# Kernel tuning notes

Measured on AMD Instinct MI355X. Metric: run time of the kernel, lower is better.

## Reference

```python
import jax, jax.numpy as jnp
import numpy as np

N_LAYERS = 8
LAYER_NAMES = ['self', 'cross'] * 4
D_MODEL = 256
NHEAD = 8
HEAD_DIM = D_MODEL // NHEAD
EPS_ATTN = 1e-6
EPS_LN = 1e-5


def _xavier(key, shape):
    fan_in, fan_out = shape[-2], shape[-1]
    limit = float(np.sqrt(6.0 / (fan_in + fan_out)))
    return jax.random.uniform(key, shape, jnp.float32, -limit, limit)


def setup_inputs() -> dict:
    key = jax.random.key(0)
    ks = jax.random.split(key, 9)
    B, L, C = 4, 4800, D_MODEL
    inp = {
        'feat0': jax.random.normal(ks[0], (B, L, C), jnp.float32),
        'feat1': jax.random.normal(ks[1], (B, L, C), jnp.float32),
        # stacked per-layer params (layers are deepcopies, independently init'd)
        'Wq': _xavier(ks[2], (N_LAYERS, C, C)),
        'Wk': _xavier(ks[3], (N_LAYERS, C, C)),
        'Wv': _xavier(ks[4], (N_LAYERS, C, C)),
        'Wm': _xavier(ks[5], (N_LAYERS, C, C)),
        'W1': _xavier(ks[6], (N_LAYERS, 2 * C, 2 * C)),
        'W2': _xavier(ks[7], (N_LAYERS, 2 * C, C)),
        'ln1_w': jnp.ones((N_LAYERS, C), jnp.float32),
        'ln1_b': jnp.zeros((N_LAYERS, C), jnp.float32),
        'ln2_w': jnp.ones((N_LAYERS, C), jnp.float32),
        'ln2_b': jnp.zeros((N_LAYERS, C), jnp.float32),
    }
    return inp


def _layernorm(x, w, b):
    mu = jnp.mean(x, axis=-1, keepdims=True)
    var = jnp.mean(jnp.square(x - mu), axis=-1, keepdims=True)
    return (x - mu) * jax.lax.rsqrt(var + EPS_LN) * w + b


def _encoder_layer(x, source, Wq, Wk, Wv, Wm, W1, W2, ln1_w, ln1_b, ln2_w, ln2_b):
    bs, L, C = x.shape
    S = source.shape[1]
    q = (x @ Wq).reshape(bs, L, NHEAD, HEAD_DIM)
    k = (source @ Wk).reshape(bs, S, NHEAD, HEAD_DIM)
    v = (source @ Wv).reshape(bs, S, NHEAD, HEAD_DIM)
    # linear (kernelized) attention: phi(x) = elu(x) + 1
    Q = jax.nn.elu(q) + 1.0
    K = jax.nn.elu(k) + 1.0
    v_len = S
    v_scaled = v / v_len
    KV = jnp.einsum('nshd,nshv->nhdv', K, v_scaled)          # [N,H,D,D]
    Z = 1.0 / (jnp.einsum('nlhd,nhd->nlh', Q, K.sum(axis=1)) + EPS_ATTN)
    msg = jnp.einsum('nlhd,nhdv,nlh->nlhv', Q, KV, Z) * v_len  # [N,L,H,D]
    msg = msg.reshape(bs, L, C) @ Wm
    msg = _layernorm(msg, ln1_w, ln1_b)
    h = jnp.concatenate([x, msg], axis=-1)                   # [N,L,2C]
    h = jnp.maximum(h @ W1, 0.0) @ W2
    h = _layernorm(h, ln2_w, ln2_b)
    return x + h


def reference(feat0, feat1, Wq, Wk, Wv, Wm, W1, W2, ln1_w, ln1_b, ln2_w, ln2_b):
    for i, name in enumerate(LAYER_NAMES):
        p = (Wq[i], Wk[i], Wv[i], Wm[i], W1[i], W2[i],
             ln1_w[i], ln1_b[i], ln2_w[i], ln2_b[i])
        if name == 'self':
            feat0 = _encoder_layer(feat0, feat0, *p)
            feat1 = _encoder_layer(feat1, feat1, *p)
        else:  # cross
            feat0 = _encoder_layer(feat0, feat1, *p)
            feat1 = _encoder_layer(feat1, feat0, *p)
    return (feat0, feat1)
```

## Files before the change

### kernel.cpp

```cpp
#include <hip/hip_runtime.h>

typedef __attribute__((ext_vector_type(8))) short short8;
typedef __attribute__((ext_vector_type(4))) float f32x4;

#define DEV static __device__ __forceinline__

DEV unsigned short f2bf(float x) {
  union { float f; unsigned int u; } c; c.f = x;
  unsigned int r = c.u + 0x7fffu + ((c.u >> 16) & 1u);
  return (unsigned short)(r >> 16);
}
DEV float bf2f(unsigned short s) {
  union { unsigned int u; float f; } c; c.u = ((unsigned int)s) << 16;
  return c.f;
}
DEV float elu1(float x) { return x > 0.f ? x + 1.f : __expf(x); }

DEV void gload_lds16(const void* g, void* l) {
  __builtin_amdgcn_global_load_lds(
      (const __attribute__((address_space(1))) unsigned int*)g,
      (__attribute__((address_space(3))) unsigned int*)l, 16, 0, 0);
}

__global__ __launch_bounds__(256)
void wprep(const float* __restrict__ src, unsigned short* __restrict__ dst,
           int K, int N, int dls) {
  const int layer = blockIdx.z;
  src += (size_t)layer * K * N;
  dst += (size_t)layer * dls;
  __shared__ float tile[64][65];
  const int n0 = blockIdx.x * 64, k0 = blockIdx.y * 64;
  const int c = threadIdx.x & 63, r4 = threadIdx.x >> 6;
#pragma unroll
  for (int i = 0; i < 16; ++i) {
    int r = (i << 2) + r4;
    tile[r][c] = src[(size_t)(k0 + r) * N + n0 + c];
  }
  __syncthreads();
#pragma unroll
  for (int i = 0; i < 16; ++i) {
    int r = (i << 2) + r4;
    dst[(size_t)(n0 + r) * K + k0 + c] = f2bf(tile[c][r]);
  }
}

__global__ __launch_bounds__(256)
void cvt_bf16(const float* __restrict__ src, unsigned short* __restrict__ dst, int n4) {
  int i = blockIdx.x * 256 + threadIdx.x;
  if (i >= n4) return;
  float4 v = ((const float4*)src)[i];
  ushort4 o;
  o.x = f2bf(v.x); o.y = f2bf(v.y); o.z = f2bf(v.z); o.w = f2bf(v.w);
  ((ushort4*)dst)[i] = o;
}

template<int EPI>
__global__ __launch_bounds__(256)
void gemm_bt(const unsigned short* __restrict__ A0,
             const unsigned short* __restrict__ A1,
             const unsigned short* __restrict__ BT,
             float* __restrict__ Cf, unsigned short* __restrict__ Cb,
             int M, int N, int K, int lda) {
  __shared__ __align__(16) unsigned short As[128 * 64];
  __shared__ __align__(16) unsigned short Bs[128 * 64];
  const int tid = threadIdx.x;
  const int lane = tid & 63, wave = tid >> 6;
  const int tn = N >> 7;
  const int bm = (int)blockIdx.x / tn, bn = (int)blockIdx.x % tn;
  const int wm = (wave >> 1) << 6, wn = (wave & 1) << 6;
  const int lr = lane & 15, lk = lane >> 4;

  f32x4 acc[4][4];
#pragma unroll
  for (int i = 0; i < 4; ++i)
#pragma unroll
    for (int j = 0; j < 4; ++j) acc[i][j] = (f32x4){0.f, 0.f, 0.f, 0.f};

  for (int k0 = 0; k0 < K; k0 += 64) {
#pragma unroll
    for (int i = 0; i < 4; ++i) {
      const int cb = (i << 2) + wave;
      const int id = (cb << 6) + lane;
      const int row = id >> 3, ck = id & 7;
      const int gk = k0 + ((ck ^ (row & 7)) << 3);
      const unsigned short* srcA;
      if (A1) {
        srcA = (gk < 256) ? (A0 + (size_t)(bm * 128 + row) * 256 + gk)
                          : (A1 + (size_t)(bm * 128 + row) * 256 + (gk - 256));
      } else {
        srcA = A0 + (size_t)(bm * 128 + row) * lda + gk;
      }
      gload_lds16(srcA, As + (size_t)cb * 512);
      const unsigned short* srcB = BT + (size_t)(bn * 128 + row) * K + gk;
      gload_lds16(srcB, Bs + (size_t)cb * 512);
    }
    __syncthreads();
#pragma unroll
    for (int kk = 0; kk < 2; ++kk) {
      short8 af[4], bfr[4];
#pragma unroll
      for (int mi = 0; mi < 4; ++mi) {
        const int row = wm + mi * 16 + lr;
        const int ck = ((kk << 2) + lk) ^ (row & 7);
        af[mi] = *(const short8*)(As + row * 64 + ck * 8);
      }
#pragma unroll
      for (int ni = 0; ni < 4; ++ni) {
        const int row = wn + ni * 16 + lr;
        const int ck = ((kk << 2) + lk) ^ (row & 7);
        bfr[ni] = *(const short8*)(Bs + row * 64 + ck * 8);
      }
#pragma unroll
      for (int mi = 0; mi < 4; ++mi)
#pragma unroll
        for (int ni = 0; ni < 4; ++ni)
          acc[mi][ni] = __builtin_amdgcn_mfma_f32_16x16x32_bf16(af[mi], bfr[ni], acc[mi][ni], 0, 0, 0);
    }
    __syncthreads();
  }

  const int cr = lk << 2;
#pragma unroll
  for (int mi = 0; mi < 4; ++mi) {
#pragma unroll
    for (int ni = 0; ni < 4; ++ni) {
      const int colbase = bn * 128 + wn + ni * 16;
      const bool kside = colbase < 256;
#pragma unroll
      for (int j = 0; j < 4; ++j) {
        const int row = bm * 128 + wm + mi * 16 + cr + j;
        const int col = colbase + lr;
        float v = acc[mi][ni][j];
        if (EPI == 0) {
          Cf[(size_t)row * N + col] = v;
        } else if (EPI == 1) {
          Cb[(size_t)row * N + col] = f2bf(fmaxf(v, 0.f));
        } else if (EPI == 2) {
          Cf[(size_t)row * N + col] = kside ? elu1(v) : v;
        } else {
          Cb[(size_t)row * N + col] = f2bf(elu1(v));
        }
      }
    }
  }
}

__global__ __launch_bounds__(256)
void kv_partial(const float* __restrict__ kv, float* __restrict__ part) {
  const int ch = blockIdx.x, h = blockIdx.y, n = blockIdx.z;
  const int t = threadIdx.x, wave = t >> 6, lane = t & 63;
  __shared__ float kb[4][8][32];
  __shared__ float vb[4][8][32];
  const int dq = lane >> 3, vq = lane & 7;
  float a[4][4];
  float ks[4] = {0.f, 0.f, 0.f, 0.f};
#pragma unroll
  for (int i = 0; i < 4; ++i)
#pragma unroll
    for (int j = 0; j < 4; ++j) a[i][j] = 0.f;

  const int s_base = ch * 480 + wave * 120;
  for (int it = 0; it < 15; ++it) {
    __syncthreads();
#pragma unroll
    for (int i = 0; i < 2; ++i) {
      int f = i * 64 + lane;
      int r = f >> 4, c4 = f & 15;
      const float* gp = kv + ((size_t)(n * 4800 + s_base + it * 8 + r)) * 512 +
                        (c4 < 8 ? h * 32 + c4 * 4 : 256 + h * 32 + (c4 - 8) * 4);
      float4 val = *(const float4*)gp;
      if (c4 < 8) *(float4*)&kb[wave][r][c4 * 4] = val;
      else        *(float4*)&vb[wave][r][(c4 - 8) * 4] = val;
    }
    __syncthreads();
#pragma unroll
    for (int si = 0; si < 8; ++si) {
      float4 kq = *(const float4*)&kb[wave][si][dq * 4];
      float4 vv = *(const float4*)&vb[wave][si][vq * 4];
      ks[0] += kq.x; ks[1] += kq.y; ks[2] += kq.z; ks[3] += kq.w;
      a[0][0] += kq.x * vv.x; a[0][1] += kq.x * vv.y; a[0][2] += kq.x * vv.z; a[0][3] += kq.x * vv.w;
      a[1][0] += kq.y * vv.x; a[1][1] += kq.y * vv.y; a[1][2] += kq.y * vv.z; a[1][3] += kq.y * vv.w;
      a[2][0] += kq.z * vv.x; a[2][1] += kq.z * vv.y; a[2][2] += kq.z * vv.z; a[2][3] += kq.z * vv.w;
      a[3][0] += kq.w * vv.x; a[3][1] += kq.w * vv.y; a[3][2] += kq.w * vv.z; a[3][3] += kq.w * vv.w;
    }
  }
  float* pb = part + ((size_t)((n * 8 + h) * 40 + ch * 4 + wave)) * 1056;
#pragma unroll
  for (int i = 0; i < 4; ++i) {
#pragma unroll
    for (int j = 0; j < 4; ++j) pb[(dq * 4 + i) * 32 + vq * 4 + j] = a[i][j];
    if (vq == 0) pb[1024 + dq * 4 + i] = ks[i];
  }
}

__global__ __launch_bounds__(256)
void kv_reduce(const float* __restrict__ part, unsigned short* __restrict__ KVb,
               float* __restrict__ Ksum) {
  const int nh = blockIdx.x, t = threadIdx.x;
  const float* pb = part + (size_t)nh * 40 * 1056;
#pragma unroll
  for (int j = 0; j < 4; ++j) {
    int e = t * 4 + j;
    float s = 0.f;
    for (int c = 0; c < 40; ++c) s += pb[c * 1056 + e];
    int dd = e >> 5, vv = e & 31;
    size_t addr = ((size_t)(nh * 2 + (vv >> 4)) * 64 + ((dd >> 3) * 16 + (vv & 15))) * 8 + (dd & 7);
    KVb[addr] = f2bf(s);
  }
  if (t < 32) {
    float s = 0.f;
    for (int c = 0; c < 40; ++c) s += pb[c * 1056 + 1024 + t];
    Ksum[nh * 32 + t] = s;
  }
}

__global__ __launch_bounds__(256)
void msg_kernel(const unsigned short* __restrict__ qb, const unsigned short* __restrict__ KVb,
                const float* __restrict__ Ksum, unsigned short* __restrict__ msg) {
  const int n = blockIdx.y;
  const int wave = threadIdx.x >> 6, lane = threadIdx.x & 63;
  const int lr = lane & 15, lk = lane >> 4;
  const int lrow = blockIdx.x * 64 + wave * 16 + lr;
  const unsigned short* qrow = qb + ((size_t)n * 4800 + lrow) * 256;
  const short8* kvv = (const short8*)KVb;
  for (int h = 0; h < 8; ++h) {
    short8 af = *(const short8*)(qrow + h * 32 + lk * 8);
    const float* ksp = Ksum + (n * 8 + h) * 32 + lk * 8;
    float zp = 0.f;
#pragma unroll
    for (int j = 0; j < 8; ++j) zp += bf2f((unsigned short)af[j]) * ksp[j];
    zp += __shfl_xor(zp, 16);
    zp += __shfl_xor(zp, 32);
    float z = 1.f / (zp + 1e-6f);
    short8 b0 = kvv[((size_t)(n * 8 + h) * 2 + 0) * 64 + lane];
    short8 b1 = kvv[((size_t)(n * 8 + h) * 2 + 1) * 64 + lane];
    f32x4 acc0 = (f32x4){0.f, 0.f, 0.f, 0.f}, acc1 = (f32x4){0.f, 0.f, 0.f, 0.f};
    acc0 = __builtin_amdgcn_mfma_f32_16x16x32_bf16(af, b0, acc0, 0, 0, 0);
    acc1 = __builtin_amdgcn_mfma_f32_16x16x32_bf16(af, b1, acc1, 0, 0, 0);
#pragma unroll
    for (int j = 0; j < 4; ++j) {
      int rr = lk * 4 + j;
      float zj = __shfl(z, rr);
      int row = blockIdx.x * 64 + wave * 16 + rr;
      size_t base = ((size_t)n * 4800 + row) * 256 + h * 32;
      msg[base + lr] = f2bf(acc0[j] * zj);
      msg[base + 16 + lr] = f2bf(acc1[j] * zj);
    }
  }
}

template<int MODE>
__global__ __launch_bounds__(256)
void ln_kernel(const float* __restrict__ in, const float* __restrict__ xres,
               const float* __restrict__ w, const float* __restrict__ b,
               float* __restrict__ outf, unsigned short* __restrict__ outb) {
  const int wave = threadIdx.x >> 6, lane = threadIdx.x & 63;
  const size_t row = (size_t)blockIdx.x * 4 + wave;
  const float4 xv = ((const float4*)(in + row * 256))[lane];
  float s = xv.x + xv.y + xv.z + xv.w;
#pragma unroll
  for (int o = 1; o < 64; o <<= 1) s += __shfl_xor(s, o);
  const float mu = s * (1.f / 256.f);
  float d0 = xv.x - mu, d1 = xv.y - mu, d2 = xv.z - mu, d3 = xv.w - mu;
  float vs = d0 * d0 + d1 * d1 + d2 * d2 + d3 * d3;
#pragma unroll
  for (int o = 1; o < 64; o <<= 1) vs += __shfl_xor(vs, o);
  const float rstd = rsqrtf(vs * (1.f / 256.f) + 1e-5f);
  const float4 wv = ((const float4*)w)[lane];
  const float4 bv = ((const float4*)b)[lane];
  float y0 = d0 * rstd * wv.x + bv.x;
  float y1 = d1 * rstd * wv.y + bv.y;
  float y2 = d2 * rstd * wv.z + bv.z;
  float y3 = d3 * rstd * wv.w + bv.w;
  if (MODE == 0) {
    ushort4 o; o.x = f2bf(y0); o.y = f2bf(y1); o.z = f2bf(y2); o.w = f2bf(y3);
    ((ushort4*)(outb + row * 256))[lane] = o;
  } else {
    const float4 xr = ((const float4*)(xres + row * 256))[lane];
    float o0 = xr.x + y0, o1 = xr.y + y1, o2 = xr.z + y2, o3 = xr.w + y3;
    ((float4*)(outf + row * 256))[lane] = make_float4(o0, o1, o2, o3);
    ushort4 ob; ob.x = f2bf(o0); ob.y = f2bf(o1); ob.z = f2bf(o2); ob.w = f2bf(o3);
    ((ushort4*)(outb + row * 256))[lane] = ob;
  }
}

extern "C" void kernel_launch(void* const* d_in, const int* in_sizes, int n_in,
                              void* d_out, int out_size, void* d_ws, size_t ws_size,
                              hipStream_t stream) {
  (void)in_sizes; (void)n_in; (void)out_size; (void)ws_size;
  const float* feat0 = (const float*)d_in[0];
  const float* feat1 = (const float*)d_in[1];
  const float* Wq = (const float*)d_in[2];
  const float* Wk = (const float*)d_in[3];
  const float* Wv = (const float*)d_in[4];
  const float* Wm = (const float*)d_in[5];
  const float* W1 = (const float*)d_in[6];
  const float* W2 = (const float*)d_in[7];
  const float* ln1w = (const float*)d_in[8];
  const float* ln1b = (const float*)d_in[9];
  const float* ln2w = (const float*)d_in[10];
  const float* ln2b = (const float*)d_in[11];

  float* F0 = (float*)d_out;
  float* F1 = F0 + (size_t)4915200;

  size_t off = 0;
  auto alloc = [&](size_t bytes) -> void* {
    void* p = (char*)d_ws + off;
    off += (bytes + 255) & ~(size_t)255;
    return p;
  };
  unsigned short* qb     = (unsigned short*)alloc((size_t)19200 * 256 * 2);
  float*          kvbuf  = (float*)alloc((size_t)19200 * 512 * 4);
  unsigned short* msgb   = (unsigned short*)alloc((size_t)19200 * 256 * 2);
  unsigned short* msglnb = (unsigned short*)alloc((size_t)19200 * 256 * 2);
  unsigned short* F0b    = (unsigned short*)alloc((size_t)19200 * 256 * 2);
  unsigned short* F1b    = (unsigned short*)alloc((size_t)19200 * 256 * 2);
  float*          part   = (float*)alloc((size_t)32 * 40 * 1056 * 4);
  unsigned short* KVb    = (unsigned short*)alloc((size_t)32768 * 2);
  float*          Ksum   = (float*)alloc((size_t)1024 * 4);
  unsigned short* WqT    = (unsigned short*)alloc((size_t)8 * 65536 * 2);
  unsigned short* WkvT   = (unsigned short*)alloc((size_t)8 * 131072 * 2);
  unsigned short* WmT    = (unsigned short*)alloc((size_t)8 * 65536 * 2);
  unsigned short* W1T    = (unsigned short*)alloc((size_t)8 * 262144 * 2);
  unsigned short* W2T    = (unsigned short*)alloc((size_t)8 * 131072 * 2);
  float* mm = kvbuf;
  float* tt = kvbuf;
  unsigned short* h1b = (unsigned short*)(kvbuf + (size_t)19200 * 256);

  hipMemcpyAsync(F0, feat0, (size_t)4915200 * 4, hipMemcpyDeviceToDevice, stream);
  hipMemcpyAsync(F1, feat1, (size_t)4915200 * 4, hipMemcpyDeviceToDevice, stream);
  cvt_bf16<<<4800, 256, 0, stream>>>(feat0, F0b, 1228800);
  cvt_bf16<<<4800, 256, 0, stream>>>(feat1, F1b, 1228800);

  wprep<<<dim3(4, 4, 8), 256, 0, stream>>>(Wq, WqT, 256, 256, 65536);
  wprep<<<dim3(4, 4, 8), 256, 0, stream>>>(Wk, WkvT, 256, 256, 131072);
  wprep<<<dim3(4, 4, 8), 256, 0, stream>>>(Wv, WkvT + 65536, 256, 256, 131072);
  wprep<<<dim3(4, 4, 8), 256, 0, stream>>>(Wm, WmT, 256, 256, 65536);
  wprep<<<dim3(8, 8, 8), 256, 0, stream>>>(W1, W1T, 512, 512, 262144);
  wprep<<<dim3(4, 8, 8), 256, 0, stream>>>(W2, W2T, 512, 256, 131072);

  auto enc = [&](float* X, unsigned short* Xb, unsigned short* Sb, int i) {
    gemm_bt<3><<<300, 256, 0, stream>>>(Xb, nullptr, WqT + (size_t)i * 65536, nullptr, qb, 19200, 256, 256, 256);
    gemm_bt<2><<<600, 256, 0, stream>>>(Sb, nullptr, WkvT + (size_t)i * 131072, kvbuf, nullptr, 19200, 512, 256, 256);
    kv_partial<<<dim3(10, 8, 4), 256, 0, stream>>>(kvbuf, part);
    kv_reduce<<<32, 256, 0, stream>>>(part, KVb, Ksum);
    msg_kernel<<<dim3(75, 4), 256, 0, stream>>>(qb, KVb, Ksum, msgb);
    gemm_bt<0><<<300, 256, 0, stream>>>(msgb, nullptr, WmT + (size_t)i * 65536, mm, nullptr, 19200, 256, 256, 256);
    ln_kernel<0><<<4800, 256, 0, stream>>>(mm, nullptr, ln1w + i * 256, ln1b + i * 256, nullptr, msglnb);
    gemm_bt<1><<<600, 256, 0, stream>>>(Xb, msglnb, W1T + (size_t)i * 262144, nullptr, h1b, 19200, 512, 512, 256);
    gemm_bt<0><<<300, 256, 0, stream>>>(h1b, nullptr, W2T + (size_t)i * 131072, tt, nullptr, 19200, 256, 512, 512);
    ln_kernel<1><<<4800, 256, 0, stream>>>(tt, X, ln2w + i * 256, ln2b + i * 256, X, Xb);
  };

  for (int i = 0; i < 8; ++i) {
    if ((i & 1) == 0) { enc(F0, F0b, F0b, i); enc(F1, F1b, F1b, i); }
    else              { enc(F0, F0b, F1b, i); enc(F1, F1b, F0b, i); }
  }
}
```

Baseline: 2.021 ms.

## Fuse LayerNorm into GEMM epilogues, batch self layers, store K/V in bf16

Adds a gemm_ln kernel that computes a full 256-wide output row tile per block and applies LayerNorm (and the residual add) in the epilogue, which removes the separate ln kernels and the fp32 intermediate round-trips. Self-attention layers now process both feature maps in one batched pass with a fused QKV GEMM (N=768). K/V are stored as bf16 instead of fp32, and the initial memcpy is folded into the bf16 conversion kernel. The trade-offs are extra reduced precision in K/V, a one-pass variance formula (E[x²]−mu²) that can lose accuracy, and larger 512-thread blocks that lower the block count for the LN-fused GEMMs.

New measurement: 1.627 ms. 19.5% less time.

```diff
diff --git a/kernel.cpp b/kernel.cpp
--- a/kernel.cpp
+++ b/kernel.cpp
@@ -45,13 +45,15 @@
 }
 
 __global__ __launch_bounds__(256)
-void cvt_bf16(const float* __restrict__ src, unsigned short* __restrict__ dst, int n4) {
+void init_feat(const float* __restrict__ src, float* __restrict__ dstf,
+               unsigned short* __restrict__ dstb, int n4) {
   int i = blockIdx.x * 256 + threadIdx.x;
   if (i >= n4) return;
   float4 v = ((const float4*)src)[i];
+  ((float4*)dstf)[i] = v;
   ushort4 o;
   o.x = f2bf(v.x); o.y = f2bf(v.y); o.z = f2bf(v.z); o.w = f2bf(v.w);
-  ((ushort4*)dst)[i] = o;
+  ((ushort4*)dstb)[i] = o;
 }
 
 template<int EPI>
@@ -59,7 +61,7 @@
 void gemm_bt(const unsigned short* __restrict__ A0,
              const unsigned short* __restrict__ A1,
              const unsigned short* __restrict__ BT,
-             float* __restrict__ Cf, unsigned short* __restrict__ Cb,
+             unsigned short* __restrict__ Cb, unsigned short* __restrict__ Cb2,
              int M, int N, int K, int lda) {
   __shared__ __align__(16) unsigned short As[128 * 64];
   __shared__ __align__(16) unsigned short Bs[128 * 64];
@@ -125,32 +127,151 @@
 #pragma unroll
     for (int ni = 0; ni < 4; ++ni) {
       const int colbase = bn * 128 + wn + ni * 16;
-      const bool kside = colbase < 256;
 #pragma unroll
       for (int j = 0; j < 4; ++j) {
         const int row = bm * 128 + wm + mi * 16 + cr + j;
         const int col = colbase + lr;
         float v = acc[mi][ni][j];
-        if (EPI == 0) {
-          Cf[(size_t)row * N + col] = v;
-        } else if (EPI == 1) {
+        if (EPI == 1) {
           Cb[(size_t)row * N + col] = f2bf(fmaxf(v, 0.f));
         } else if (EPI == 2) {
-          Cf[(size_t)row * N + col] = kside ? elu1(v) : v;
+          Cb[(size_t)row * N + col] = f2bf(colbase < 256 ? elu1(v) : v);
+        } else if (EPI == 3) {
+          Cb[(size_t)row * 256 + col] = f2bf(elu1(v));
         } else {
-          Cb[(size_t)row * N + col] = f2bf(elu1(v));
+          if (colbase < 256) Cb[(size_t)row * 256 + col] = f2bf(elu1(v));
+          else Cb2[(size_t)row * 512 + (col - 256)] = f2bf(colbase < 512 ? elu1(v) : v);
         }
       }
     }
   }
 }
 
-__global__ __launch_bounds__(256)
-void kv_partial(const float* __restrict__ kv, float* __restrict__ part) {
+template<int EPI>
+__global__ __launch_bounds__(512)
+void gemm_ln(const unsigned short* __restrict__ A, const unsigned short* __restrict__ BT,
+             const float* __restrict__ lnw, const float* __restrict__ lnb,
+             const float* __restrict__ xres, float* __restrict__ outf,
+             unsigned short* __restrict__ outb, int K) {
+  __shared__ __align__(16) unsigned short As[128 * 64];
+  __shared__ __align__(16) unsigned short Bs[256 * 64];
+  const int tid = threadIdx.x;
+  const int lane = tid & 63, wid = tid >> 6;
+  const int bm = blockIdx.x;
+  const int wm = (wid >> 2) << 6, wn = (wid & 3) << 6;
+  const int lr = lane & 15, lk = lane >> 4;
+
+  f32x4 acc[4][4];
+#pragma unroll
+  for (int i = 0; i < 4; ++i)
+#pragma unroll
+    for (int j = 0; j < 4; ++j) acc[i][j] = (f32x4){0.f, 0.f, 0.f, 0.f};
+
+  for (int k0 = 0; k0 < K; k0 += 64) {
+#pragma unroll
+    for (int i = 0; i < 2; ++i) {
+      const int cb = i * 8 + wid;
+      const int id = (cb << 6) + lane;
+      const int row = id >> 3, ck = id & 7;
+      const int gk = k0 + ((ck ^ (row & 7)) << 3);
+      gload_lds16(A + (size_t)(bm * 128 + row) * K + gk, As + (size_t)cb * 512);
+    }
+#pragma unroll
+    for (int i = 0; i < 4; ++i) {
+      const int cb = i * 8 + wid;
+      const int id = (cb << 6) + lane;
+      const int row = id >> 3, ck = id & 7;
+      const int gk = k0 + ((ck ^ (row & 7)) << 3);
+      gload_lds16(BT + (size_t)row * K + gk, Bs + (size_t)cb * 512);
+    }
+    __syncthreads();
+#pragma unroll
+    for (int kk = 0; kk < 2; ++kk) {
+      short8 af[4], bfr[4];
+#pragma unroll
+      for (int mi = 0; mi < 4; ++mi) {
+        const int row = wm + mi * 16 + lr;
+        const int ck = ((kk << 2) + lk) ^ (row & 7);
+        af[mi] = *(const short8*)(As + row * 64 + ck * 8);
+      }
+#pragma unroll
+      for (int ni = 0; ni < 4; ++ni) {
+        const int row = wn + ni * 16 + lr;
+        const int ck = ((kk << 2) + lk) ^ (row & 7);
+        bfr[ni] = *(const short8*)(Bs + row * 64 + ck * 8);
+      }
+#pragma unroll
+      for (int mi = 0; mi < 4; ++mi)
+#pragma unroll
+        for (int ni = 0; ni < 4; ++ni)
+          acc[mi][ni] = __builtin_amdgcn_mfma_f32_16x16x32_bf16(af[mi], bfr[ni], acc[mi][ni], 0, 0, 0);
+    }
+    __syncthreads();
+  }
+
+  float* red = (float*)As;
+  float wv[4], bv[4];
+#pragma unroll
+  for (int ni = 0; ni < 4; ++ni) {
+    wv[ni] = lnw[wn + ni * 16 + lr];
+    bv[ni] = lnb[wn + ni * 16 + lr];
+  }
+#pragma unroll
+  for (int mi = 0; mi < 4; ++mi) {
+#pragma unroll
+    for (int j = 0; j < 4; ++j) {
+      float s = 0.f, q = 0.f;
+#pragma unroll
+      for (int ni = 0; ni < 4; ++ni) {
+        float v = acc[mi][ni][j];
+        s += v; q += v * v;
+      }
+#pragma unroll
+      for (int o = 1; o < 16; o <<= 1) {
+        s += __shfl_xor(s, o);
+        q += __shfl_xor(q, o);
+      }
+      if (lr == 0) {
+        int row = wm + mi * 16 + (lk << 2) + j;
+        red[row * 8 + (wid & 3) * 2] = s;
+        red[row * 8 + (wid & 3) * 2 + 1] = q;
+      }
+    }
+  }
+  __syncthreads();
+#pragma unroll
+  for (int mi = 0; mi < 4; ++mi) {
+#pragma unroll
+    for (int j = 0; j < 4; ++j) {
+      const int row = wm + mi * 16 + (lk << 2) + j;
+      const size_t grow = (size_t)bm * 128 + row;
+      float s = red[row * 8] + red[row * 8 + 2] + red[row * 8 + 4] + red[row * 8 + 6];
+      float q = red[row * 8 + 1] + red[row * 8 + 3] + red[row * 8 + 5] + red[row * 8 + 7];
+      float mu = s * (1.f / 256.f);
+      float var = q * (1.f / 256.f) - mu * mu;
+      float rstd = rsqrtf(var + 1e-5f);
+#pragma unroll
+      for (int ni = 0; ni < 4; ++ni) {
+        int col = wn + ni * 16 + lr;
+        float y = (acc[mi][ni][j] - mu) * rstd * wv[ni] + bv[ni];
+        if (EPI == 0) {
+          outb[grow * 256 + col] = f2bf(y);
+        } else {
+          float o = xres[grow * 256 + col] + y;
+          outf[grow * 256 + col] = o;
+          outb[grow * 256 + col] = f2bf(o);
+        }
+      }
+    }
+  }
+}
+
+__global__ __launch_bounds__(256)
+void kv_partial(const unsigned short* __restrict__ kvb, float* __restrict__ part) {
   const int ch = blockIdx.x, h = blockIdx.y, n = blockIdx.z;
   const int t = threadIdx.x, wave = t >> 6, lane = t & 63;
-  __shared__ float kb[4][8][32];
-  __shared__ float vb[4][8][32];
+  __shared__ float kb[4][8][36];
+  __shared__ float vb[4][8][36];
   const int dq = lane >> 3, vq = lane & 7;
   float a[4][4];
   float ks[4] = {0.f, 0.f, 0.f, 0.f};
@@ -160,18 +281,16 @@
     for (int j = 0; j < 4; ++j) a[i][j] = 0.f;
 
   const int s_base = ch * 480 + wave * 120;
+  const int half = lane >> 5, l = lane & 31, r = l >> 2, c8 = l & 3;
+  const unsigned short* src = kvb + ((size_t)n * 4800 + s_base + r) * 512 +
+                              half * 256 + h * 32 + c8 * 8;
+  float* dst = (half ? &vb[wave][r][0] : &kb[wave][r][0]) + c8 * 8;
+
   for (int it = 0; it < 15; ++it) {
     __syncthreads();
-#pragma unroll
-    for (int i = 0; i < 2; ++i) {
-      int f = i * 64 + lane;
-      int r = f >> 4, c4 = f & 15;
-      const float* gp = kv + ((size_t)(n * 4800 + s_base + it * 8 + r)) * 512 +
-                        (c4 < 8 ? h * 32 + c4 * 4 : 256 + h * 32 + (c4 - 8) * 4);
-      float4 val = *(const float4*)gp;
-      if (c4 < 8) *(float4*)&kb[wave][r][c4 * 4] = val;
-      else        *(float4*)&vb[wave][r][(c4 - 8) * 4] = val;
-    }
+    short8 raw = *(const short8*)(src + (size_t)it * 8 * 512);
+#pragma unroll
+    for (int e = 0; e < 8; ++e) dst[e] = bf2f((unsigned short)raw[e]);
     __syncthreads();
 #pragma unroll
     for (int si = 0; si < 8; ++si) {
@@ -246,41 +365,6 @@
       msg[base + lr] = f2bf(acc0[j] * zj);
       msg[base + 16 + lr] = f2bf(acc1[j] * zj);
     }
-  }
-}
-
-template<int MODE>
-__global__ __launch_bounds__(256)
-void ln_kernel(const float* __restrict__ in, const float* __restrict__ xres,
-               const float* __restrict__ w, const float* __restrict__ b,
-               float* __restrict__ outf, unsigned short* __restrict__ outb) {
-  const int wave = threadIdx.x >> 6, lane = threadIdx.x & 63;
-  const size_t row = (size_t)blockIdx.x * 4 + wave;
-  const float4 xv = ((const float4*)(in + row * 256))[lane];
-  float s = xv.x + xv.y + xv.z + xv.w;
-#pragma unroll
-  for (int o = 1; o < 64; o <<= 1) s += __shfl_xor(s, o);
-  const float mu = s * (1.f / 256.f);
-  float d0 = xv.x - mu, d1 = xv.y - mu, d2 = xv.z - mu, d3 = xv.w - mu;
-  float vs = d0 * d0 + d1 * d1 + d2 * d2 + d3 * d3;
-#pragma unroll
-  for (int o = 1; o < 64; o <<= 1) vs += __shfl_xor(vs, o);
-  const float rstd = rsqrtf(vs * (1.f / 256.f) + 1e-5f);
-  const float4 wv = ((const float4*)w)[lane];
-  const float4 bv = ((const float4*)b)[lane];
-  float y0 = d0 * rstd * wv.x + bv.x;
-  float y1 = d1 * rstd * wv.y + bv.y;
-  float y2 = d2 * rstd * wv.z + bv.z;
-  float y3 = d3 * rstd * wv.w + bv.w;
-  if (MODE == 0) {
-    ushort4 o; o.x = f2bf(y0); o.y = f2bf(y1); o.z = f2bf(y2); o.w = f2bf(y3);
-    ((ushort4*)(outb + row * 256))[lane] = o;
-  } else {
-    const float4 xr = ((const float4*)(xres + row * 256))[lane];
-    float o0 = xr.x + y0, o1 = xr.y + y1, o2 = xr.z + y2, o3 = xr.w + y3;
-    ((float4*)(outf + row * 256))[lane] = make_float4(o0, o1, o2, o3);
-    ushort4 ob; ob.x = f2bf(o0); ob.y = f2bf(o1); ob.z = f2bf(o2); ob.w = f2bf(o3);
-    ((ushort4*)(outb + row * 256))[lane] = ob;
   }
 }
 
@@ -310,51 +394,72 @@
     off += (bytes + 255) & ~(size_t)255;
     return p;
   };
-  unsigned short* qb     = (unsigned short*)alloc((size_t)19200 * 256 * 2);
-  float*          kvbuf  = (float*)alloc((size_t)19200 * 512 * 4);
-  unsigned short* msgb   = (unsigned short*)alloc((size_t)19200 * 256 * 2);
-  unsigned short* msglnb = (unsigned short*)alloc((size_t)19200 * 256 * 2);
-  unsigned short* F0b    = (unsigned short*)alloc((size_t)19200 * 256 * 2);
-  unsigned short* F1b    = (unsigned short*)alloc((size_t)19200 * 256 * 2);
-  float*          part   = (float*)alloc((size_t)32 * 40 * 1056 * 4);
-  unsigned short* KVb    = (unsigned short*)alloc((size_t)32768 * 2);
-  float*          Ksum   = (float*)alloc((size_t)1024 * 4);
-  unsigned short* WqT    = (unsigned short*)alloc((size_t)8 * 65536 * 2);
-  unsigned short* WkvT   = (unsigned short*)alloc((size_t)8 * 131072 * 2);
+  unsigned short* Fb     = (unsigned short*)alloc((size_t)38400 * 256 * 2);
+  unsigned short* qb     = (unsigned short*)alloc((size_t)38400 * 256 * 2);
+  unsigned short* kvb    = (unsigned short*)alloc((size_t)38400 * 512 * 2);
+  unsigned short* msgb   = (unsigned short*)alloc((size_t)38400 * 256 * 2);
+  unsigned short* msglnb = (unsigned short*)alloc((size_t)38400 * 256 * 2);
+  float*          part   = (float*)alloc((size_t)64 * 40 * 1056 * 4);
+  unsigned short* KVb    = (unsigned short*)alloc((size_t)65536 * 2);
+  float*          Ksum   = (float*)alloc((size_t)2048 * 4);
+  unsigned short* WqkvT  = (unsigned short*)alloc((size_t)8 * 196608 * 2);
   unsigned short* WmT    = (unsigned short*)alloc((size_t)8 * 65536 * 2);
   unsigned short* W1T    = (unsigned short*)alloc((size_t)8 * 262144 * 2);
   unsigned short* W2T    = (unsigned short*)alloc((size_t)8 * 131072 * 2);
-  float* mm = kvbuf;
-  float* tt = kvbuf;
-  unsigned short* h1b = (unsigned short*)(kvbuf + (size_t)19200 * 256);
-
-  hipMemcpyAsync(F0, feat0, (size_t)4915200 * 4, hipMemcpyDeviceToDevice, stream);
-  hipMemcpyAsync(F1, feat1, (size_t)4915200 * 4, hipMemcpyDeviceToDevice, stream);
-  cvt_bf16<<<4800, 256, 0, stream>>>(feat0, F0b, 1228800);
-  cvt_bf16<<<4800, 256, 0, stream>>>(feat1, F1b, 1228800);
-
-  wprep<<<dim3(4, 4, 8), 256, 0, stream>>>(Wq, WqT, 256, 256, 65536);
-  wprep<<<dim3(4, 4, 8), 256, 0, stream>>>(Wk, WkvT, 256, 256, 131072);
-  wprep<<<dim3(4, 4, 8), 256, 0, stream>>>(Wv, WkvT + 65536, 256, 256, 131072);
+  unsigned short* h1b = kvb;
+  unsigned short* F0b = Fb;
+  unsigned short* F1b = Fb + (size_t)19200 * 256;
+
+  init_feat<<<4800, 256, 0, stream>>>(feat0, F0, F0b, 1228800);
+  init_feat<<<4800, 256, 0, stream>>>(feat1, F1, F1b, 1228800);
+
+  wprep<<<dim3(4, 4, 8), 256, 0, stream>>>(Wq, WqkvT, 256, 256, 196608);
+  wprep<<<dim3(4, 4, 8), 256, 0, stream>>>(Wk, WqkvT + 65536, 256, 256, 196608);
+  wprep<<<dim3(4, 4, 8), 256, 0, stream>>>(Wv, WqkvT + 131072, 256, 256, 196608);
   wprep<<<dim3(4, 4, 8), 256, 0, stream>>>(Wm, WmT, 256, 256, 65536);
   wprep<<<dim3(8, 8, 8), 256, 0, stream>>>(W1, W1T, 512, 512, 262144);
   wprep<<<dim3(4, 8, 8), 256, 0, stream>>>(W2, W2T, 512, 256, 131072);
 
-  auto enc = [&](float* X, unsigned short* Xb, unsigned short* Sb, int i) {
-    gemm_bt<3><<<300, 256, 0, stream>>>(Xb, nullptr, WqT + (size_t)i * 65536, nullptr, qb, 19200, 256, 256, 256);
-    gemm_bt<2><<<600, 256, 0, stream>>>(Sb, nullptr, WkvT + (size_t)i * 131072, kvbuf, nullptr, 19200, 512, 256, 256);
-    kv_partial<<<dim3(10, 8, 4), 256, 0, stream>>>(kvbuf, part);
+  auto enc_self = [&](int i) {
+    gemm_bt<4><<<1800, 256, 0, stream>>>(Fb, nullptr, WqkvT + (size_t)i * 196608,
+                                         qb, kvb, 38400, 768, 256, 256);
+    kv_partial<<<dim3(10, 8, 8), 256, 0, stream>>>(kvb, part);
+    kv_reduce<<<64, 256, 0, stream>>>(part, KVb, Ksum);
+    msg_kernel<<<dim3(75, 8), 256, 0, stream>>>(qb, KVb, Ksum, msgb);
+    gemm_ln<0><<<300, 512, 0, stream>>>(msgb, WmT + (size_t)i * 65536,
+                                        ln1w + i * 256, ln1b + i * 256,
+                                        nullptr, nullptr, msglnb, 256);
+    gemm_bt<1><<<1200, 256, 0, stream>>>(Fb, msglnb, W1T + (size_t)i * 262144,
+                                         h1b, nullptr, 38400, 512, 512, 256);
+    gemm_ln<1><<<300, 512, 0, stream>>>(h1b, W2T + (size_t)i * 131072,
+                                        ln2w + i * 256, ln2b + i * 256,
+                                        F0, F0, Fb, 512);
+  };
+
+  auto enc_cross = [&](float* X, unsigned short* Xb, unsigned short* Sb, int i) {
+    gemm_bt<3><<<300, 256, 0, stream>>>(Xb, nullptr, WqkvT + (size_t)i * 196608,
+                                        qb, nullptr, 19200, 256, 256, 256);
+    gemm_bt<2><<<600, 256, 0, stream>>>(Sb, nullptr, WqkvT + (size_t)i * 196608 + 65536,
+                                        kvb, nullptr, 19200, 512, 256, 256);
+    kv_partial<<<dim3(10, 8, 4), 256, 0, stream>>>(kvb, part);
     kv_reduce<<<32, 256, 0, stream>>>(part, KVb, Ksum);
     msg_kernel<<<dim3(75, 4), 256, 0, stream>>>(qb, KVb, Ksum, msgb);
-    gemm_bt<0><<<300, 256, 0, stream>>>(msgb, nullptr, WmT + (size_t)i * 65536, mm, nullptr, 19200, 256, 256, 256);
-    ln_kernel<0><<<4800, 256, 0, stream>>>(mm, nullptr, ln1w + i * 256, ln1b + i * 256, nullptr, msglnb);
-    gemm_bt<1><<<600, 256, 0, stream>>>(Xb, msglnb, W1T + (size_t)i * 262144, nullptr, h1b, 19200, 512, 512, 256);
-    gemm_bt<0><<<300, 256, 0, stream>>>(h1b, nullptr, W2T + (size_t)i * 131072, tt, nullptr, 19200, 256, 512, 512);
-    ln_kernel<1><<<4800, 256, 0, stream>>>(tt, X, ln2w + i * 256, ln2b + i * 256, X, Xb);
+    gemm_ln<0><<<150, 512, 0, stream>>>(msgb, WmT + (size_t)i * 65536,
+                                        ln1w + i * 256, ln1b + i * 256,
+                                        nullptr, nullptr, msglnb, 256);
+    gemm_bt<1><<<600, 256, 0, stream>>>(Xb, msglnb, W1T + (size_t)i * 262144,
+                                        h1b, nullptr, 19200, 512, 512, 256);
+    gemm_ln<1><<<150, 512, 0, stream>>>(h1b, W2T + (size_t)i * 131072,
+                                        ln2w + i * 256, ln2b + i * 256,
+                                        X, X, Xb, 512);
   };
 
   for (int i = 0; i < 8; ++i) {
-    if ((i & 1) == 0) { enc(F0, F0b, F0b, i); enc(F1, F1b, F1b, i); }
-    else              { enc(F0, F0b, F1b, i); enc(F1, F1b, F0b, i); }
-  }
-}
+    if ((i & 1) == 0) {
+      enc_self(i);
+    } else {
+      enc_cross(F0, F0b, F1b, i);
+      enc_cross(F1, F1b, F0b, i);
+    }
+  }
+}
```
